# Performance work log

Measured on AMD Instinct MI355X. Metric: run time of the kernel, lower is better.

## Reference

```python
import jax, jax.numpy as jnp
import numpy as np

V, L, NP, NC, D, S, NNEG = 2, 2, 120000, 120000, 128, 100, 50
TEMP = 0.5


def setup_inputs() -> dict:
    key = jax.random.key(0)
    ks = jax.random.split(key, 10)
    return {
        'emb_p': jax.random.normal(ks[0], (V, L, NP, D), dtype=jnp.float32),
        'emb_c': jax.random.normal(ks[1], (V, L, NC, D), dtype=jnp.float32),
        'W1': jax.random.normal(ks[2], (D, D), dtype=jnp.float32) * (1.0 / np.sqrt(D)),
        'b1': jax.random.normal(ks[3], (D,), dtype=jnp.float32) * 0.01,
        'W2': jax.random.normal(ks[4], (D, D), dtype=jnp.float32) * (1.0 / np.sqrt(D)),
        'b2': jax.random.normal(ks[5], (D,), dtype=jnp.float32) * 0.01,
        'idx_p': jax.random.randint(ks[6], (V, L, S), 0, NP, dtype=jnp.int64),
        'idx_c': jax.random.randint(ks[7], (V, L, S), 0, NC, dtype=jnp.int64),
        'neg_idx_p': jax.random.randint(ks[8], (V, L, S, NNEG), 0, NC, dtype=jnp.int64),
        'neg_idx_c': jax.random.randint(ks[9], (V, L, S, NNEG), 0, NP, dtype=jnp.int64),
    }


def _l2norm(x):
    return x / jnp.maximum(jnp.linalg.norm(x, axis=-1, keepdims=True), 1e-12)


def _type_loss(Pz_self, Pz_other, idx, neg_idx):
    total = jnp.float32(0.0)
    for vi in range(V):
        for li in range(L):
            ids = idx[vi, li]                      # [S]
            z = Pz_self[vi, li][ids]               # [S,D] anchor projections
            # positives: same node index, all other (view,layer) keys (3 when V=L=2)
            pos_keys = [(1 - vi, li), (vi, 1 - li), (1 - vi, 1 - li)]
            pos = jnp.stack([Pz_self[vj, lj][ids] for vj, lj in pos_keys])  # [3,S,D]
            pos_sim = jnp.exp(jnp.einsum('sd,ksd->ks', z, pos) / TEMP).sum(0)  # [S]
            # within-type negatives: other sampled anchors (exclude self position)
            sims = jnp.exp(z @ z.T / TEMP)         # [S,S]
            neg_within = sims.sum(1) - jnp.diagonal(sims)
            # cross-type negatives: 50 sampled per anchor from other type, same key
            ng = Pz_other[vi, li][neg_idx[vi, li]]  # [S,NNEG,D]
            neg_cross = jnp.exp(jnp.einsum('sd,snd->sn', z, ng) / TEMP).sum(1)
            neg = neg_within + neg_cross
            total = total + (-jnp.log(pos_sim / (pos_sim + neg))).sum()
    return total


def reference(emb_p, emb_c, W1, b1, W2, b2, idx_p, idx_c, neg_idx_p, neg_idx_c):
    def project(x):
        return jnp.maximum(x @ W1 + b1, 0.0) @ W2 + b2
    Pz_p = _l2norm(project(emb_p))  # [V,L,NP,D]
    Pz_c = _l2norm(project(emb_c))  # [V,L,NC,D]
    total = _type_loss(Pz_p, Pz_c, idx_p, neg_idx_p) + _type_loss(Pz_c, Pz_p, idx_c, neg_idx_c)
    total_samples = 2 * V * L * S
    return total / jnp.float32(total_samples)
```

## Files before the change

kernel.cpp:

```cpp
#include <hip/hip_runtime.h>
#include <hip/hip_bf16.h>
#include <math.h>

#define NNODE 120000
#define DDIM  128
#define SS    100
#define NNEGS 50
#define ROWS_A 1600
#define ROWS_N 20000
#define TOTAL_ROWS 43200
#define BLK_ROWS 256
#define NBLK 169
#define HSTRIDE 136
#define INV_TEMP 2.0f

typedef unsigned short ushort_t;
typedef __attribute__((ext_vector_type(8))) short bf16x8;
typedef __attribute__((ext_vector_type(8))) unsigned short u16x8;
typedef __attribute__((ext_vector_type(4))) float f32x4;

__device__ __forceinline__ ushort_t f2b(float f) {
  __hip_bfloat16 h = __float2bfloat16(f);
  return *reinterpret_cast<ushort_t*>(&h);
}
__device__ __forceinline__ float b2f(ushort_t h) {
  return __builtin_bit_cast(float, (unsigned)h << 16);
}
__device__ __forceinline__ bool idx_is64(const void* p) {
  const unsigned* q = (const unsigned*)p;
  return (q[1] | q[3] | q[5] | q[7]) == 0u;
}
__device__ __forceinline__ int ld_idx(const void* p, int i, bool is64) {
  return is64 ? (int)((const long long*)p)[i] : ((const int*)p)[i];
}

__device__ __forceinline__ const float* row_src(
    int rid, bool is64,
    const float* emb_p, const float* emb_c,
    const void* idx_p, const void* idx_c,
    const void* nidx_p, const void* nidx_c)
{
  if (rid < 2 * ROWS_A) {
    const int typ = rid / ROWS_A;
    const int rr  = rid - typ * ROWS_A;
    const int slice = rr / 400;
    const int rem   = rr - slice * 400;
    const int node  = ld_idx(typ ? idx_c : idx_p, rem, is64);
    return (typ ? emb_c : emb_p) + ((size_t)slice * NNODE + node) * DDIM;
  } else {
    const int r2  = rid - 2 * ROWS_A;
    const int typ = r2 / ROWS_N;
    const int rr  = r2 - typ * ROWS_N;
    const int slice = rr / (SS * NNEGS);
    const int rem   = rr - slice * (SS * NNEGS);
    const int node  = ld_idx(typ ? nidx_c : nidx_p, slice * (SS * NNEGS) + rem, is64);
    return (typ ? emb_p : emb_c) + ((size_t)slice * NNODE + node) * DDIM;
  }
}

__global__ __launch_bounds__(512, 1)
void proj_kernel(const float* __restrict__ emb_p, const float* __restrict__ emb_c,
                 const float* __restrict__ W1, const float* __restrict__ b1v,
                 const float* __restrict__ W2, const float* __restrict__ b2v,
                 const void* __restrict__ idx_p, const void* __restrict__ idx_c,
                 const void* __restrict__ nidx_p, const void* __restrict__ nidx_c,
                 ushort_t* __restrict__ zout, float* __restrict__ out)
{
  __shared__ __align__(16) ushort_t wlds[2 * 16384];
  __shared__ __align__(16) ushort_t slab[BLK_ROWS * HSTRIDE];
  const int t = threadIdx.x, w = t >> 6, l = t & 63;
  const int g = l >> 4, li = l & 15;
  const bool is64 = idx_is64(idx_p);
  const int base = blockIdx.x * BLK_ROWS;
  const int ra = w * 32 + li;
  const int rb = ra + 16;

  if (blockIdx.x == 0 && t == 0) out[0] = 0.f;

  int rida = base + ra, ridb = base + rb;
  if (rida > TOTAL_ROWS - 1) rida = TOTAL_ROWS - 1;
  if (ridb > TOTAL_ROWS - 1) ridb = TOTAL_ROWS - 1;
  const float* sa = row_src(rida, is64, emb_p, emb_c, idx_p, idx_c, nidx_p, nidx_c);
  const float* sb = row_src(ridb, is64, emb_p, emb_c, idx_p, idx_c, nidx_p, nidx_c);
  bf16x8 afa[4], afb[4];
  #pragma unroll
  for (int kc = 0; kc < 4; ++kc) {
    const float4 a0 = *(const float4*)(sa + kc * 32 + g * 8);
    const float4 a1 = *(const float4*)(sa + kc * 32 + g * 8 + 4);
    const float4 b0 = *(const float4*)(sb + kc * 32 + g * 8);
    const float4 b1 = *(const float4*)(sb + kc * 32 + g * 8 + 4);
    bf16x8 fa, fb;
    fa[0]=(short)f2b(a0.x); fa[1]=(short)f2b(a0.y); fa[2]=(short)f2b(a0.z); fa[3]=(short)f2b(a0.w);
    fa[4]=(short)f2b(a1.x); fa[5]=(short)f2b(a1.y); fa[6]=(short)f2b(a1.z); fa[7]=(short)f2b(a1.w);
    fb[0]=(short)f2b(b0.x); fb[1]=(short)f2b(b0.y); fb[2]=(short)f2b(b0.z); fb[3]=(short)f2b(b0.w);
    fb[4]=(short)f2b(b1.x); fb[5]=(short)f2b(b1.y); fb[6]=(short)f2b(b1.z); fb[7]=(short)f2b(b1.w);
    afa[kc] = fa; afb[kc] = fb;
  }

  #pragma unroll
  for (int p = 0; p < 8; ++p) {
    const int s = p * 512 + t;
    const int layer = s >> 11;
    const int idx = s & 2047;
    const int lane = idx & 63, kcct = idx >> 6;
    const int kc = kcct >> 3, ct = kcct & 7;
    const float* W = layer ? W2 : W1;
    const float* wp = W + (size_t)(kc * 32 + ((lane >> 4) << 3)) * DDIM
                        + ct * 16 + (lane & 15);
    u16x8 v;
    #pragma unroll
    for (int e = 0; e < 8; ++e) v[e] = f2b(wp[(size_t)e * DDIM]);
    *(u16x8*)&wlds[(size_t)s * 8] = v;
  }
  __syncthreads();

  f32x4 aa[8], ab[8];
  #pragma unroll
  for (int ct = 0; ct < 8; ++ct) {
    const float bv = b1v[ct * 16 + li];
    aa[ct] = (f32x4){bv, bv, bv, bv};
    ab[ct] = aa[ct];
  }
  #pragma unroll
  for (int kc = 0; kc < 4; ++kc)
    #pragma unroll
    for (int ct = 0; ct < 8; ++ct) {
      const bf16x8 bf = *(const bf16x8*)&wlds[((kc * 8 + ct) * 64 + l) * 8];
      aa[ct] = __builtin_amdgcn_mfma_f32_16x16x32_bf16(afa[kc], bf, aa[ct], 0, 0, 0);
      ab[ct] = __builtin_amdgcn_mfma_f32_16x16x32_bf16(afb[kc], bf, ab[ct], 0, 0, 0);
    }
  #pragma unroll
  for (int rg = 0; rg < 4; ++rg) {
    ushort_t* rowpa = &slab[(w * 32 + 4 * g + rg) * HSTRIDE + li];
    ushort_t* rowpb = rowpa + 16 * HSTRIDE;
    #pragma unroll
    for (int ct = 0; ct < 8; ++ct) {
      rowpa[ct * 16] = f2b(fmaxf(aa[ct][rg], 0.f));
      rowpb[ct * 16] = f2b(fmaxf(ab[ct][rg], 0.f));
    }
  }
  #pragma unroll
  for (int ct = 0; ct < 8; ++ct) {
    const float bv = b2v[ct * 16 + li];
    aa[ct] = (f32x4){bv, bv, bv, bv};
    ab[ct] = aa[ct];
  }
  {
    const ushort_t* rowa = &slab[(w * 32 + li) * HSTRIDE + g * 8];
    const ushort_t* rowb = rowa + 16 * HSTRIDE;
    #pragma unroll
    for (int kc = 0; kc < 4; ++kc) {
      const bf16x8 hfa = *(const bf16x8*)(rowa + kc * 32);
      const bf16x8 hfb = *(const bf16x8*)(rowb + kc * 32);
      #pragma unroll
      for (int ct = 0; ct < 8; ++ct) {
        const bf16x8 bf = *(const bf16x8*)&wlds[16384 + ((kc * 8 + ct) * 64 + l) * 8];
        aa[ct] = __builtin_amdgcn_mfma_f32_16x16x32_bf16(hfa, bf, aa[ct], 0, 0, 0);
        ab[ct] = __builtin_amdgcn_mfma_f32_16x16x32_bf16(hfb, bf, ab[ct], 0, 0, 0);
      }
    }
  }
  #pragma unroll
  for (int grp = 0; grp < 2; ++grp) {
    f32x4* ac = grp ? ab : aa;
    float sc[4];
    #pragma unroll
    for (int rg = 0; rg < 4; ++rg) {
      float ssq = 0.f;
      #pragma unroll
      for (int ct = 0; ct < 8; ++ct) ssq += ac[ct][rg] * ac[ct][rg];
      ssq += __shfl_xor(ssq, 1);
      ssq += __shfl_xor(ssq, 2);
      ssq += __shfl_xor(ssq, 4);
      ssq += __shfl_xor(ssq, 8);
      sc[rg] = 1.f / fmaxf(sqrtf(ssq), 1e-12f);
    }
    #pragma unroll
    for (int rg = 0; rg < 4; ++rg) {
      ushort_t* rowp = &slab[(w * 32 + grp * 16 + 4 * g + rg) * HSTRIDE + li];
      #pragma unroll
      for (int ct = 0; ct < 8; ++ct)
        rowp[ct * 16] = f2b(ac[ct][rg] * sc[rg]);
    }
  }
  {
    uint4* d4 = (uint4*)(zout + (size_t)(base + w * 32) * DDIM);
    const uint4* s4 = (const uint4*)slab;
    #pragma unroll
    for (int i = 0; i < 8; ++i) {
      const int e = l + 64 * i;
      const int row = e >> 4, c = e & 15;
      d4[e] = s4[(w * 32 + row) * (HSTRIDE / 8) + c];
    }
  }
}

#define LROW_U4 17
__global__ __launch_bounds__(512)
void loss_kernel(const ushort_t* __restrict__ zb, float* __restrict__ out)
{
  __shared__ __align__(16) uint4 sl[SS * LROW_U4];
  __shared__ float sterm[8];
  const int bid = blockIdx.x;
  const int grp = bid & 7;
  const int chunk = bid >> 3;
  const int typ = grp >> 2;
  const int vl  = grp & 3;
  const ushort_t* A  = zb + (size_t)(typ ? ROWS_A : 0) * DDIM;
  const ushort_t* Nb = zb + (size_t)(2 * ROWS_A + (typ ? ROWS_N : 0)) * DDIM;
  const ushort_t* SL = A + (size_t)(vl * 4 + vl) * SS * DDIM;
  const int t = threadIdx.x, l = t & 63, w = t >> 6;
  const int tsub = l >> 3, eg = l & 7;
  const int s_raw = chunk * 8 + w;
  const bool act = (s_raw < SS);
  const int s = act ? s_raw : SS - 1;

  #pragma unroll
  for (int i = 0; i < 4; ++i) {
    const int c = i * 512 + t;
    if (c < SS * 16)
      sl[(c >> 4) * LROW_U4 + (c & 15)] = ((const uint4*)SL)[c];
  }

  const ushort_t* zs = SL + (size_t)s * DDIM;
  float zr[16];
  {
    const u16x8 v0 = *(const u16x8*)(zs + eg * 16);
    const u16x8 v1 = *(const u16x8*)(zs + eg * 16 + 8);
    #pragma unroll
    for (int j = 0; j < 8; ++j) { zr[j] = b2f(v0[j]); zr[j + 8] = b2f(v1[j]); }
  }

  float pe = 0.f, ne = 0.f;
  #pragma unroll
  for (int pass = 0; pass < 6; ++pass) {
    const int n = pass * 8 + tsub;
    const ushort_t* tp = Nb + (size_t)((vl * SS + s) * NNEGS + n) * DDIM;
    const u16x8 x0 = *(const u16x8*)(tp + eg * 16);
    const u16x8 x1 = *(const u16x8*)(tp + eg * 16 + 8);
    float d = 0.f;
    #pragma unroll
    for (int j = 0; j < 8; ++j) {
      d = fmaf(b2f(x0[j]), zr[j], d);
      d = fmaf(b2f(x1[j]), zr[j + 8], d);
    }
    d += __shfl_xor(d, 1);
    d += __shfl_xor(d, 2);
    d += __shfl_xor(d, 4);
    ne += __expf(d * INV_TEMP);
  }
  __syncthreads();

  #pragma unroll
  for (int pass = 6; pass < 19; ++pass) {
    const int tt = pass * 8 + tsub;
    float d = 0.f;
    bool is_pos = false;
    if (tt >= 53) {
      int j = tt - 53;
      int t2 = j + (j >= s ? 1 : 0);
      const uint4* rp = &sl[t2 * LROW_U4 + eg * 2];
      const u16x8 x0 = *(const u16x8*)rp;
      const u16x8 x1 = *(const u16x8*)(rp + 1);
      #pragma unroll
      for (int j2 = 0; j2 < 8; ++j2) {
        d = fmaf(b2f(x0[j2]), zr[j2], d);
        d = fmaf(b2f(x1[j2]), zr[j2 + 8], d);
      }
    } else {
      const ushort_t* tp;
      if (tt < 50) {
        tp = Nb + (size_t)((vl * SS + s) * NNEGS + tt) * DDIM;
      } else {
        const int kp = tt - 50;
        const int k = kp + (kp >= vl ? 1 : 0);
        tp = A + (size_t)((k * 4 + vl) * SS + s) * DDIM;
        is_pos = true;
      }
      const u16x8 x0 = *(const u16x8*)(tp + eg * 16);
      const u16x8 x1 = *(const u16x8*)(tp + eg * 16 + 8);
      #pragma unroll
      for (int j2 = 0; j2 < 8; ++j2) {
        d = fmaf(b2f(x0[j2]), zr[j2], d);
        d = fmaf(b2f(x1[j2]), zr[j2 + 8], d);
      }
    }
    d += __shfl_xor(d, 1);
    d += __shfl_xor(d, 2);
    d += __shfl_xor(d, 4);
    const float e = __expf(d * INV_TEMP);
    if (is_pos) pe += e; else ne += e;
  }
  pe += __shfl_xor(pe, 8);  ne += __shfl_xor(ne, 8);
  pe += __shfl_xor(pe, 16); ne += __shfl_xor(ne, 16);
  pe += __shfl_xor(pe, 32); ne += __shfl_xor(ne, 32);
  if (l == 0) sterm[w] = act ? -logf(pe / (pe + ne)) : 0.f;
  __syncthreads();
  if (t == 0) {
    float tot = 0.f;
    #pragma unroll
    for (int i = 0; i < 8; ++i) tot += sterm[i];
    atomicAdd(out, tot * (1.0f / 800.0f));
  }
}

extern "C" void kernel_launch(void* const* d_in, const int* in_sizes, int n_in,
                              void* d_out, int out_size, void* d_ws, size_t ws_size,
                              hipStream_t stream) {
  const float* emb_p = (const float*)d_in[0];
  const float* emb_c = (const float*)d_in[1];
  const float* W1    = (const float*)d_in[2];
  const float* b1    = (const float*)d_in[3];
  const float* W2    = (const float*)d_in[4];
  const float* b2    = (const float*)d_in[5];
  const void*  idx_p  = d_in[6];
  const void*  idx_c  = d_in[7];
  const void*  nidx_p = d_in[8];
  const void*  nidx_c = d_in[9];
  float* out = (float*)d_out;
  ushort_t* zrows = (ushort_t*)d_ws;

  proj_kernel<<<NBLK, 512, 0, stream>>>(
      emb_p, emb_c, W1, b1, W2, b2, idx_p, idx_c, nidx_p, nidx_c, zrows, out);
  loss_kernel<<<104, 512, 0, stream>>>(zrows, out);
}
```

Before: 28.12 us.

## Precompute bf16 weight fragments in a separate kernel and halve proj block size

Adds a small kernel that converts W1/W2 into bf16 MFMA fragment layout once and stores it in workspace. The projection kernel then reads B fragments straight from global memory (L2-cached) instead of having every block convert and stage 64 KB of weights in LDS. It also runs 338 blocks of 256 threads instead of 169 of 512, which drops the block-wide barrier and spreads work over more CUs. The trade-off is an extra kernel launch and weight operands fetched from global/L2 rather than LDS on every MFMA.

Result: slower. 34.00 us (+20.9%).

```diff
diff --git a/kernel.cpp b/kernel.cpp
--- a/kernel.cpp
+++ b/kernel.cpp
@@ -9,8 +9,9 @@
 #define ROWS_A 1600
 #define ROWS_N 20000
 #define TOTAL_ROWS 43200
-#define BLK_ROWS 256
-#define NBLK 169
+#define NBLK 338
+#define ZPAD_BYTES (43264 * 256)
+#define WFRAG_SHORTS 16384
 #define HSTRIDE 136
 #define INV_TEMP 2.0f
 
@@ -58,26 +59,40 @@
   }
 }
 
-__global__ __launch_bounds__(512, 1)
+__global__ __launch_bounds__(64)
+void wfrag_kernel(const float* __restrict__ W1, const float* __restrict__ W2,
+                  ushort_t* __restrict__ wfrag, float* __restrict__ out)
+{
+  if (blockIdx.x == 0 && threadIdx.x == 0) out[0] = 0.f;
+  const int b = blockIdx.x;
+  const int layer = b >> 5, kc = (b >> 3) & 3, ct = b & 7;
+  const int l = threadIdx.x;
+  const float* W = layer ? W2 : W1;
+  ushort_t* dst = wfrag + layer * WFRAG_SHORTS + (size_t)((kc * 8 + ct) * 64 + l) * 8;
+  const int col   = ct * 16 + (l & 15);
+  const int krow0 = kc * 32 + ((l >> 4) << 3);
+  #pragma unroll
+  for (int e = 0; e < 8; ++e)
+    dst[e] = f2b(W[(size_t)(krow0 + e) * DDIM + col]);
+}
+
+__global__ __launch_bounds__(256)
 void proj_kernel(const float* __restrict__ emb_p, const float* __restrict__ emb_c,
-                 const float* __restrict__ W1, const float* __restrict__ b1v,
-                 const float* __restrict__ W2, const float* __restrict__ b2v,
+                 const float* __restrict__ b1v, const float* __restrict__ b2v,
                  const void* __restrict__ idx_p, const void* __restrict__ idx_c,
                  const void* __restrict__ nidx_p, const void* __restrict__ nidx_c,
-                 ushort_t* __restrict__ zout, float* __restrict__ out)
+                 const ushort_t* __restrict__ wfrag,
+                 ushort_t* __restrict__ zout)
 {
-  __shared__ __align__(16) ushort_t wlds[2 * 16384];
-  __shared__ __align__(16) ushort_t slab[BLK_ROWS * HSTRIDE];
+  __shared__ __align__(16) ushort_t slab[4 * 32 * HSTRIDE];
   const int t = threadIdx.x, w = t >> 6, l = t & 63;
   const int g = l >> 4, li = l & 15;
   const bool is64 = idx_is64(idx_p);
-  const int base = blockIdx.x * BLK_ROWS;
-  const int ra = w * 32 + li;
-  const int rb = ra + 16;
-
-  if (blockIdx.x == 0 && t == 0) out[0] = 0.f;
-
-  int rida = base + ra, ridb = base + rb;
+  const int base = blockIdx.x * 128;
+  ushort_t* slw = &slab[w * 32 * HSTRIDE];
+
+  int rida = base + w * 32 + li;
+  int ridb = rida + 16;
   if (rida > TOTAL_ROWS - 1) rida = TOTAL_ROWS - 1;
   if (ridb > TOTAL_ROWS - 1) ridb = TOTAL_ROWS - 1;
   const float* sa = row_src(rida, is64, emb_p, emb_c, idx_p, idx_c, nidx_p, nidx_c);
@@ -97,23 +112,6 @@
     afa[kc] = fa; afb[kc] = fb;
   }
 
-  #pragma unroll
-  for (int p = 0; p < 8; ++p) {
-    const int s = p * 512 + t;
-    const int layer = s >> 11;
-    const int idx = s & 2047;
-    const int lane = idx & 63, kcct = idx >> 6;
-    const int kc = kcct >> 3, ct = kcct & 7;
-    const float* W = layer ? W2 : W1;
-    const float* wp = W + (size_t)(kc * 32 + ((lane >> 4) << 3)) * DDIM
-                        + ct * 16 + (lane & 15);
-    u16x8 v;
-    #pragma unroll
-    for (int e = 0; e < 8; ++e) v[e] = f2b(wp[(size_t)e * DDIM]);
-    *(u16x8*)&wlds[(size_t)s * 8] = v;
-  }
-  __syncthreads();
-
   f32x4 aa[8], ab[8];
   #pragma unroll
   for (int ct = 0; ct < 8; ++ct) {
@@ -125,13 +123,13 @@
   for (int kc = 0; kc < 4; ++kc)
     #pragma unroll
     for (int ct = 0; ct < 8; ++ct) {
-      const bf16x8 bf = *(const bf16x8*)&wlds[((kc * 8 + ct) * 64 + l) * 8];
+      const bf16x8 bf = *(const bf16x8*)&wfrag[((kc * 8 + ct) * 64 + l) * 8];
       aa[ct] = __builtin_amdgcn_mfma_f32_16x16x32_bf16(afa[kc], bf, aa[ct], 0, 0, 0);
       ab[ct] = __builtin_amdgcn_mfma_f32_16x16x32_bf16(afb[kc], bf, ab[ct], 0, 0, 0);
     }
   #pragma unroll
   for (int rg = 0; rg < 4; ++rg) {
-    ushort_t* rowpa = &slab[(w * 32 + 4 * g + rg) * HSTRIDE + li];
+    ushort_t* rowpa = &slw[(4 * g + rg) * HSTRIDE + li];
     ushort_t* rowpb = rowpa + 16 * HSTRIDE;
     #pragma unroll
     for (int ct = 0; ct < 8; ++ct) {
@@ -146,7 +144,7 @@
     ab[ct] = aa[ct];
   }
   {
-    const ushort_t* rowa = &slab[(w * 32 + li) * HSTRIDE + g * 8];
+    const ushort_t* rowa = &slw[li * HSTRIDE + g * 8];
     const ushort_t* rowb = rowa + 16 * HSTRIDE;
     #pragma unroll
     for (int kc = 0; kc < 4; ++kc) {
@@ -154,7 +152,7 @@
       const bf16x8 hfb = *(const bf16x8*)(rowb + kc * 32);
       #pragma unroll
       for (int ct = 0; ct < 8; ++ct) {
-        const bf16x8 bf = *(const bf16x8*)&wlds[16384 + ((kc * 8 + ct) * 64 + l) * 8];
+        const bf16x8 bf = *(const bf16x8*)&wfrag[WFRAG_SHORTS + ((kc * 8 + ct) * 64 + l) * 8];
         aa[ct] = __builtin_amdgcn_mfma_f32_16x16x32_bf16(hfa, bf, aa[ct], 0, 0, 0);
         ab[ct] = __builtin_amdgcn_mfma_f32_16x16x32_bf16(hfb, bf, ab[ct], 0, 0, 0);
       }
@@ -177,7 +175,7 @@
     }
     #pragma unroll
     for (int rg = 0; rg < 4; ++rg) {
-      ushort_t* rowp = &slab[(w * 32 + grp * 16 + 4 * g + rg) * HSTRIDE + li];
+      ushort_t* rowp = &slw[(grp * 16 + 4 * g + rg) * HSTRIDE + li];
       #pragma unroll
       for (int ct = 0; ct < 8; ++ct)
         rowp[ct * 16] = f2b(ac[ct][rg] * sc[rg]);
@@ -185,12 +183,12 @@
   }
   {
     uint4* d4 = (uint4*)(zout + (size_t)(base + w * 32) * DDIM);
-    const uint4* s4 = (const uint4*)slab;
+    const uint4* s4 = (const uint4*)slw;
     #pragma unroll
     for (int i = 0; i < 8; ++i) {
       const int e = l + 64 * i;
       const int row = e >> 4, c = e & 15;
-      d4[e] = s4[(w * 32 + row) * (HSTRIDE / 8) + c];
+      d4[e] = s4[row * (HSTRIDE / 8) + c];
     }
   }
 }
@@ -319,8 +317,10 @@
   const void*  nidx_c = d_in[9];
   float* out = (float*)d_out;
   ushort_t* zrows = (ushort_t*)d_ws;
-
-  proj_kernel<<<NBLK, 512, 0, stream>>>(
-      emb_p, emb_c, W1, b1, W2, b2, idx_p, idx_c, nidx_p, nidx_c, zrows, out);
+  ushort_t* wfrag = (ushort_t*)((char*)d_ws + ZPAD_BYTES);
+
+  wfrag_kernel<<<64, 64, 0, stream>>>(W1, W2, wfrag, out);
+  proj_kernel<<<NBLK, 256, 0, stream>>>(
+      emb_p, emb_c, b1, b2, idx_p, idx_c, nidx_p, nidx_c, wfrag, zrows);
   loss_kernel<<<104, 512, 0, stream>>>(zrows, out);
 }
```
